# Kernel tuning notes

Measured on AMD Instinct MI355X. Metric: run time of the kernel, lower is better.

## Reference

```python
import jax, jax.numpy as jnp
import numpy as np

USER_NUM = 100000
ITEM_NUM = 50000
EMBED = 64
N_LAYERS = 3
E_RATE = 2000000
E_TRUST = 500000
E_PRED = 100000


def setup_inputs() -> dict:
    key = jax.random.key(0)
    ks = jax.random.split(key, 10)
    return {
        "emb_user": jax.random.normal(ks[0], (USER_NUM, EMBED), dtype=jnp.float32),
        "emb_item": jax.random.normal(ks[1], (ITEM_NUM, EMBED), dtype=jnp.float32),
        "rate_u": jax.random.randint(ks[2], (E_RATE,), 0, USER_NUM, dtype=jnp.int32),
        "rate_i": jax.random.randint(ks[3], (E_RATE,), 0, ITEM_NUM, dtype=jnp.int32),
        "trust_src": jax.random.randint(ks[4], (E_TRUST,), 0, USER_NUM, dtype=jnp.int32),
        "trust_dst": jax.random.randint(ks[5], (E_TRUST,), 0, USER_NUM, dtype=jnp.int32),
        "pos_u": jax.random.randint(ks[6], (E_PRED,), 0, USER_NUM, dtype=jnp.int32),
        "pos_i": jax.random.randint(ks[7], (E_PRED,), 0, ITEM_NUM, dtype=jnp.int32),
        "neg_u": jax.random.randint(ks[8], (E_PRED,), 0, USER_NUM, dtype=jnp.int32),
        "neg_i": jax.random.randint(ks[9], (E_PRED,), 0, ITEM_NUM, dtype=jnp.int32),
    }


def _degrees(idx, n):
    # float degree counts, clamped to >=1 (DGL GraphConv clamps zero degrees)
    d = jax.ops.segment_sum(jnp.ones_like(idx, dtype=jnp.float32), idx, num_segments=n)
    return jnp.maximum(d, 1.0)


def _gcn_conv(h_src, src, dst, n_dst, deg_src, deg_dst):
    # GraphConv(norm='both', weight=False, bias=False):
    # out[v] = deg(v)^-1/2 * sum_{u->v} deg(u)^-1/2 * h[u]
    ns = jax.lax.rsqrt(deg_src)
    nd = jax.lax.rsqrt(deg_dst)
    msg = (h_src * ns[:, None])[src]          # [E, D] gather
    agg = jax.ops.segment_sum(msg, dst, num_segments=n_dst)
    return agg * nd[:, None]


def reference(emb_user, emb_item, rate_u, rate_i, trust_src, trust_dst,
              pos_u, pos_i, neg_u, neg_i):
    nU, nI = emb_user.shape[0], emb_item.shape[0]
    deg_u = _degrees(rate_u, nU)       # user degree in rate graph (out for rate, in for rated-by)
    deg_i = _degrees(rate_i, nI)       # item degree in rate graph
    deg_ts = _degrees(trust_src, nU)
    deg_td = _degrees(trust_dst, nU)

    res_u, res_i = emb_user, emb_item
    cur_u, cur_i = emb_user, emb_item
    for _ in range(N_LAYERS):
        # item -> user ('rated-by'): src deg = deg_i, dst deg = deg_u
        new_u = _gcn_conv(cur_i, rate_i, rate_u, nU, deg_i, deg_u)
        # user -> item ('rate')
        new_i = _gcn_conv(cur_u, rate_u, rate_i, nI, deg_u, deg_i)
        # user -> user ('trust'), added into user output
        new_u = new_u + _gcn_conv(cur_u, trust_src, trust_dst, nU, deg_ts, deg_td)
        res_u = res_u + new_u
        res_i = res_i + new_i
        cur_u, cur_i = new_u, new_i

    scale = 1.0 / (N_LAYERS + 1)
    res_u = res_u * scale
    res_i = res_i * scale

    # HeteroDotProductPredictor on 'rate' etype: u_dot_v -> [E, 1]
    pos_score = jnp.sum(res_u[pos_u] * res_i[pos_i], axis=-1, keepdims=True)
    neg_score = jnp.sum(res_u[neg_u] * res_i[neg_i], axis=-1, keepdims=True)
    return pos_score, neg_score
```

## Files before the change

### kernel.cpp

```cpp
#include <hip/hip_runtime.h>
#include <hip/hip_fp16.h>

#define NU 100000
#define NI 50000
#define D  64
#define CAPU 64
#define CAPI 96
#define CAPT 32
#define BS 256

#define NB1 256
#define KPB1 391
#define CAPB1 9216
#define NB2 256
#define KPB2 196
#define CAPB2 9216
#define NB3 128
#define KPB3 782
#define CAPB3 4864
#define NB4 128
#define CAPB4 4864
#define GR 224
#define GT 32

typedef unsigned long long u64;

__global__ void __launch_bounds__(1024) k_binAll(
    const int* __restrict__ ru, const int* __restrict__ ri,
    const int* __restrict__ ts, const int* __restrict__ td,
    int* __restrict__ bc1, int* __restrict__ bc2,
    int* __restrict__ bc3, int* __restrict__ bc4,
    u64* __restrict__ bins1, u64* __restrict__ bins2,
    u64* __restrict__ bins3, u64* __restrict__ bins4,
    int E_rate, int E_trust)
{
    __shared__ int cnt[512];
    __shared__ int base[512];
    int b = blockIdx.x, tid = threadIdx.x;
    if (b < GR) {
        if (tid < 512) cnt[tid] = 0;
        __syncthreads();
        for (int c0 = b * 1024; c0 < E_rate; c0 += GR * 1024) {
            int e = c0 + tid;
            if (e < E_rate) {
                int u = ru[e], it = ri[e];
                atomicAdd(&cnt[u / KPB1], 1);
                atomicAdd(&cnt[256 + it / KPB2], 1);
            }
        }
        __syncthreads();
        if (tid < 256)      base[tid] = atomicAdd(&bc1[tid], cnt[tid]);
        else if (tid < 512) base[tid] = atomicAdd(&bc2[tid - 256], cnt[tid]);
        __syncthreads();
        if (tid < 512) cnt[tid] = 0;
        __syncthreads();
        for (int c0 = b * 1024; c0 < E_rate; c0 += GR * 1024) {
            int e = c0 + tid;
            if (e < E_rate) {
                int u = ru[e], it = ri[e];
                int b1 = u / KPB1, b2 = it / KPB2;
                int r1 = atomicAdd(&cnt[b1], 1);
                int o1 = base[b1] + r1;
                if (o1 < CAPB1) bins1[(size_t)b1 * CAPB1 + o1] = ((u64)u << 32) | (unsigned)it;
                int r2 = atomicAdd(&cnt[256 + b2], 1);
                int o2 = base[256 + b2] + r2;
                if (o2 < CAPB2) bins2[(size_t)b2 * CAPB2 + o2] = ((u64)it << 32) | (unsigned)u;
            }
        }
    } else {
        int bb = b - GR;
        if (tid < 256) cnt[tid] = 0;
        __syncthreads();
        for (int c0 = bb * 1024; c0 < E_trust; c0 += GT * 1024) {
            int e = c0 + tid;
            if (e < E_trust) {
                int s = ts[e], dd = td[e];
                atomicAdd(&cnt[dd / KPB3], 1);
                atomicAdd(&cnt[128 + s / KPB3], 1);
            }
        }
        __syncthreads();
        if (tid < 128)      base[tid] = atomicAdd(&bc3[tid], cnt[tid]);
        else if (tid < 256) base[tid] = atomicAdd(&bc4[tid - 128], cnt[tid]);
        __syncthreads();
        if (tid < 256) cnt[tid] = 0;
        __syncthreads();
        for (int c0 = bb * 1024; c0 < E_trust; c0 += GT * 1024) {
            int e = c0 + tid;
            if (e < E_trust) {
                int s = ts[e], dd = td[e];
                int b3 = dd / KPB3, b4 = s / KPB3;
                int r3 = atomicAdd(&cnt[b3], 1);
                int o3 = base[b3] + r3;
                if (o3 < CAPB3) bins3[(size_t)b3 * CAPB3 + o3] = ((u64)dd << 32) | (unsigned)s;
                int r4 = atomicAdd(&cnt[128 + b4], 1);
                int o4 = base[128 + b4] + r4;
                if (o4 < CAPB4) bins4[(size_t)b4 * CAPB4 + o4] = ((u64)s << 32);
            }
        }
    }
}

__global__ void __launch_bounds__(512) k_buildAll(
    const u64* __restrict__ bins1, const u64* __restrict__ bins2,
    const u64* __restrict__ bins3, const u64* __restrict__ bins4,
    const int* __restrict__ bc1, const int* __restrict__ bc2,
    const int* __restrict__ bc3, const int* __restrict__ bc4,
    int* __restrict__ colU, int* __restrict__ colI, int* __restrict__ colT,
    int* __restrict__ degU, int* __restrict__ degI,
    int* __restrict__ degT, int* __restrict__ degS)
{
    __shared__ int cnt[KPB3];
    int b = blockIdx.x, tid = threadIdx.x;
    const u64* bins; int n, k0, kpb, colcap, nmax; int* col; int* deg;
    if (b < NB1) {
        bins = bins1 + (size_t)b * CAPB1; n = bc1[b]; if (n > CAPB1) n = CAPB1;
        k0 = b * KPB1; kpb = KPB1; colcap = CAPU; col = colU; deg = degU; nmax = NU;
    } else if (b < NB1 + NB2) {
        int q = b - NB1;
        bins = bins2 + (size_t)q * CAPB2; n = bc2[q]; if (n > CAPB2) n = CAPB2;
        k0 = q * KPB2; kpb = KPB2; colcap = CAPI; col = colI; deg = degI; nmax = NI;
    } else if (b < NB1 + NB2 + NB3) {
        int q = b - NB1 - NB2;
        bins = bins3 + (size_t)q * CAPB3; n = bc3[q]; if (n > CAPB3) n = CAPB3;
        k0 = q * KPB3; kpb = KPB3; colcap = CAPT; col = colT; deg = degT; nmax = NU;
    } else {
        int q = b - NB1 - NB2 - NB3;
        bins = bins4 + (size_t)q * CAPB4; n = bc4[q]; if (n > CAPB4) n = CAPB4;
        k0 = q * KPB3; kpb = KPB3; colcap = 0; col = nullptr; deg = degS; nmax = NU;
    }
    for (int t = tid; t < kpb; t += 512) cnt[t] = 0;
    __syncthreads();
    if (col) {
        for (int i = tid; i < n; i += 512) {
            u64 e = bins[i];
            int k = (int)(e >> 32);
            int v = (int)(e & 0xffffffffu);
            int c = atomicAdd(&cnt[k - k0], 1);
            if (c < colcap) col[(size_t)k * colcap + c] = v;
        }
    } else {
        for (int i = tid; i < n; i += 512) {
            int k = (int)(bins[i] >> 32);
            atomicAdd(&cnt[k - k0], 1);
        }
    }
    __syncthreads();
    for (int t = tid; t < kpb; t += 512) {
        int k = k0 + t;
        if (k < nmax) {
            int c = cnt[t];
            if (colcap && c > colcap) c = colcap;
            deg[k] = c;
        }
    }
}

__global__ void k_degrs(const int* __restrict__ degU, const int* __restrict__ degI,
                        const int* __restrict__ degT, const int* __restrict__ degS,
                        float* __restrict__ rs_u, float* __restrict__ rs_i,
                        float* __restrict__ rs_td, float* __restrict__ rs_tsu) {
    int i = blockIdx.x * blockDim.x + threadIdx.x;
    if (i < NU) {
        int a = degU[i]; float ru = rsqrtf((float)(a < 1 ? 1 : a));
        rs_u[i] = ru;
        int b = degT[i]; rs_td[i] = rsqrtf((float)(b < 1 ? 1 : b));
        int c = degS[i]; rs_tsu[i] = rsqrtf((float)(c < 1 ? 1 : c)) / ru;
    }
    if (i < NI) {
        int a = degI[i]; rs_i[i] = rsqrtf((float)(a < 1 ? 1 : a));
    }
}

__device__ __forceinline__ uint2 pack4(float a, float b, float c, float d) {
    __half2 lo = __floats2half2_rn(a, b);
    __half2 hi = __floats2half2_rn(c, d);
    uint2 r;
    r.x = *(unsigned*)&lo;
    r.y = *(unsigned*)&hi;
    return r;
}

__global__ void k_inith(const float* __restrict__ src, const float* __restrict__ rs,
                        uint2* __restrict__ curS, uint2* __restrict__ res, int n16) {
    int i = blockIdx.x * blockDim.x + threadIdx.x;
    if (i >= n16) return;
    float4 v = ((const float4*)src)[i];
    float s = rs[i >> 4];
    res[i]  = pack4(v.x, v.y, v.z, v.w);
    curS[i] = pack4(s * v.x, s * v.y, s * v.z, s * v.w);
}

__global__ void k_zrow(uint2* uA, uint2* uB, uint2* iA, uint2* iB) {
    int t = threadIdx.x;
    int e = t & 15;
    uint2 z; z.x = 0; z.y = 0;
    if (t < 16)      uA[(size_t)NU * 16 + e] = z;
    else if (t < 32) uB[(size_t)NU * 16 + e] = z;
    else if (t < 48) iA[(size_t)NI * 16 + e] = z;
    else             iB[(size_t)NI * 16 + e] = z;
}

__global__ void k_layer(const int* __restrict__ colU, const int* __restrict__ degU,
                        const int* __restrict__ colT, const int* __restrict__ degT,
                        const int* __restrict__ colI, const int* __restrict__ degI,
                        const float* __restrict__ rs_u, const float* __restrict__ rs_i,
                        const float* __restrict__ rs_td, const float* __restrict__ rs_tsu,
                        const uint2* __restrict__ cuR, const uint2* __restrict__ ciS,
                        uint2* __restrict__ nuR, uint2* __restrict__ niS,
                        uint2* __restrict__ resu, uint2* __restrict__ resi) {
    int b = blockIdx.x;
    int m = b % 3;
    int base = b / 3;
    int wid = threadIdx.x >> 6;
    int lane = threadIdx.x & 63;
    int grp = lane >> 4;
    int gl  = lane & 15;
    if (m < 2) {
        int node = ((base * 2 + m) * 4 + wid) * 4 + grp;
        if (node >= NU) return;
        float4 acc = {0.f, 0.f, 0.f, 0.f};
        {
            int bb = node * CAPU, e = bb + degU[node];
            for (int k0 = bb; k0 < e; k0 += 16) {
                int idx = k0 + gl;
                int n = idx < e ? colU[idx] : NI;
                #pragma unroll
                for (int j = 0; j < 16; ++j) {
                    int nn = __shfl(n, j, 16);
                    uint2 q = ciS[(size_t)nn * 16 + gl];
                    float2 f = __half22float2(*(__half2*)&q.x);
                    float2 g = __half22float2(*(__half2*)&q.y);
                    acc.x += f.x; acc.y += f.y; acc.z += g.x; acc.w += g.y;
                }
            }
        }
        float4 acc2 = {0.f, 0.f, 0.f, 0.f};
        {
            int bb = node * CAPT, e = bb + degT[node];
            int sub = gl & 7;
            for (int k0 = bb; k0 < e; k0 += 8) {
                int idx = k0 + sub;
                int n = idx < e ? colT[idx] : NU;
                float w = idx < e ? rs_tsu[n] : 0.f;
                #pragma unroll
                for (int j = 0; j < 8; ++j) {
                    int nn  = __shfl(n, j, 16);
                    float ww = __shfl(w, j, 16);
                    uint2 q = cuR[(size_t)nn * 16 + gl];
                    float2 f = __half22float2(*(__half2*)&q.x);
                    float2 g = __half22float2(*(__half2*)&q.y);
                    acc2.x += ww * f.x; acc2.y += ww * f.y;
                    acc2.z += ww * g.x; acc2.w += ww * g.y;
                }
            }
        }
        float su = rs_u[node], st = rs_td[node];
        float vx = su * acc.x + st * acc2.x;
        float vy = su * acc.y + st * acc2.y;
        float vz = su * acc.z + st * acc2.z;
        float vw = su * acc.w + st * acc2.w;
        size_t o = (size_t)node * 16 + gl;
        nuR[o] = pack4(su * vx, su * vy, su * vz, su * vw);
        uint2 r = resu[o];
        float2 ra = __half22float2(*(__half2*)&r.x);
        float2 rb = __half22float2(*(__half2*)&r.y);
        resu[o] = pack4(ra.x + vx, ra.y + vy, rb.x + vz, rb.y + vw);
    } else {
        int node = (base * 4 + wid) * 4 + grp;
        if (node >= NI) return;
        float4 acc = {0.f, 0.f, 0.f, 0.f};
        {
            int bb = node * CAPI, e = bb + degI[node];
            for (int k0 = bb; k0 < e; k0 += 16) {
                int idx = k0 + gl;
                int n = idx < e ? colI[idx] : NU;
                #pragma unroll
                for (int j = 0; j < 16; ++j) {
                    int nn = __shfl(n, j, 16);
                    uint2 q = cuR[(size_t)nn * 16 + gl];
                    float2 f = __half22float2(*(__half2*)&q.x);
                    float2 g = __half22float2(*(__half2*)&q.y);
                    acc.x += f.x; acc.y += f.y; acc.z += g.x; acc.w += g.y;
                }
            }
        }
        float si = rs_i[node];
        float vx = si * acc.x, vy = si * acc.y, vz = si * acc.z, vw = si * acc.w;
        size_t o = (size_t)node * 16 + gl;
        niS[o] = pack4(si * vx, si * vy, si * vz, si * vw);
        uint2 r = resi[o];
        float2 ra = __half22float2(*(__half2*)&r.x);
        float2 rb = __half22float2(*(__half2*)&r.y);
        resi[o] = pack4(ra.x + vx, ra.y + vy, rb.x + vz, rb.y + vw);
    }
}

__global__ void k_pred(const int* __restrict__ pu, const int* __restrict__ pi,
                       const int* __restrict__ nuv, const int* __restrict__ niv,
                       const __half2* __restrict__ ru, const __half2* __restrict__ ri,
                       float* __restrict__ out, int E) {
    long long tid = (long long)blockIdx.x * blockDim.x + threadIdx.x;
    int e = (int)(tid >> 4);
    int c2 = ((int)tid & 15) * 2;
    if (e >= 2 * E) return;
    int ee = (e < E) ? e : e - E;
    int u  = (e < E) ? pu[ee] : nuv[ee];
    int it = (e < E) ? pi[ee] : niv[ee];
    float2 a0 = __half22float2(ru[(size_t)u  * 32 + c2]);
    float2 a1 = __half22float2(ru[(size_t)u  * 32 + c2 + 1]);
    float2 b0 = __half22float2(ri[(size_t)it * 32 + c2]);
    float2 b1 = __half22float2(ri[(size_t)it * 32 + c2 + 1]);
    float s = a0.x * b0.x + a0.y * b0.y + a1.x * b1.x + a1.y * b1.y;
    s += __shfl_xor(s, 1); s += __shfl_xor(s, 2);
    s += __shfl_xor(s, 4); s += __shfl_xor(s, 8);
    if (((int)tid & 15) == 0) out[e] = s * (1.0f / 16.0f);
}

extern "C" void kernel_launch(void* const* d_in, const int* in_sizes, int n_in,
                              void* d_out, int out_size, void* d_ws, size_t ws_size,
                              hipStream_t stream) {
    const float* emb_u  = (const float*)d_in[0];
    const float* emb_i  = (const float*)d_in[1];
    const int* rate_u   = (const int*)d_in[2];
    const int* rate_i   = (const int*)d_in[3];
    const int* trust_s  = (const int*)d_in[4];
    const int* trust_d  = (const int*)d_in[5];
    const int* pos_u    = (const int*)d_in[6];
    const int* pos_i    = (const int*)d_in[7];
    const int* neg_u    = (const int*)d_in[8];
    const int* neg_i    = (const int*)d_in[9];
    const int E_rate  = in_sizes[2];
    const int E_trust = in_sizes[4];
    const int E_pred  = in_sizes[6];

    int* iw   = (int*)d_ws;
    int* degU = iw;
    int* degI = degU + NU;
    int* degT = degI + NI;
    int* degS = degT + NU;
    int* bc1  = degS + NU;
    int* bc2  = bc1 + NB1;
    int* bc3  = bc2 + NB2;
    int* bc4  = bc3 + NB3;
    int* colU = bc4 + NB4;
    int* colI = colU + (size_t)NU * CAPU;
    int* colT = colI + (size_t)NI * CAPI;
    float* rs_u   = (float*)(colT + (size_t)NU * CAPT);
    float* rs_i   = rs_u  + NU;
    float* rs_td  = rs_i  + NI;
    float* rs_tsu = rs_td + NU;
    uint2* uRA  = (uint2*)(rs_tsu + NU);
    uint2* uRB  = uRA + (size_t)(NU + 1) * 16;
    uint2* iSA  = uRB + (size_t)(NU + 1) * 16;
    uint2* iSB  = iSA + (size_t)(NI + 1) * 16;
    uint2* res_u = iSB + (size_t)(NI + 1) * 16;
    uint2* res_i = res_u + (size_t)NU * 16;
    u64* bins1 = (u64*)uRA;
    u64* bins2 = bins1 + (size_t)NB1 * CAPB1;
    u64* bins3 = bins2 + (size_t)NB2 * CAPB2;
    u64* bins4 = bins3 + (size_t)NB3 * CAPB3;

    hipMemsetAsync(bc1, 0, (NB1 + NB2 + NB3 + NB4) * sizeof(int), stream);

    k_binAll<<<GR + GT, 1024, 0, stream>>>(rate_u, rate_i, trust_s, trust_d,
                                           bc1, bc2, bc3, bc4,
                                           bins1, bins2, bins3, bins4,
                                           E_rate, E_trust);
    k_buildAll<<<NB1 + NB2 + NB3 + NB4, 512, 0, stream>>>(
        bins1, bins2, bins3, bins4, bc1, bc2, bc3, bc4,
        colU, colI, colT, degU, degI, degT, degS);

    k_degrs<<<(NU + BS - 1) / BS, BS, 0, stream>>>(degU, degI, degT, degS,
                                                   rs_u, rs_i, rs_td, rs_tsu);

    k_inith<<<(NU * 16 + BS - 1) / BS, BS, 0, stream>>>(emb_u, rs_u, uRA, res_u, NU * 16);
    k_inith<<<(NI * 16 + BS - 1) / BS, BS, 0, stream>>>(emb_i, rs_i, iSA, res_i, NI * 16);
    k_zrow<<<1, 64, 0, stream>>>(uRA, uRB, iSA, iSB);

    uint2* cu = uRA; uint2* nu_ = uRB;
    uint2* ci = iSA; uint2* ni_ = iSB;
    for (int l = 0; l < 3; ++l) {
        k_layer<<<9375, BS, 0, stream>>>(colU, degU, colT, degT, colI, degI,
                                         rs_u, rs_i, rs_td, rs_tsu,
                                         cu, ci, nu_, ni_, res_u, res_i);
        uint2* t;
        t = cu; cu = nu_; nu_ = t;
        t = ci; ci = ni_; ni_ = t;
    }

    long long tp = (long long)2 * E_pred * 16;
    k_pred<<<(unsigned)((tp + BS - 1) / BS), BS, 0, stream>>>(
        pos_u, pos_i, neg_u, neg_i, (const __half2*)res_u, (const __half2*)res_i,
        (float*)d_out, E_pred);
}
```

Baseline: 366.3 us.

## Split embeddings into column halves and process layers per half

Reorganises the fp16 node feature arrays into two 32-column halves stored as separate planes. Each layer now runs separate user and item kernels per half, so every gather touches a smaller working set that is more likely to stay in cache. Bin entries are packed into 32-bit words instead of 64-bit, and rating-neighbour sums accumulate in half2 instead of fp32. This trades more launches and repeated index reads for better locality, at the cost of lower accumulation precision.

Result: slower. 465.7 us (+27.1%).

```diff
diff --git a/kernel.cpp b/kernel.cpp
--- a/kernel.cpp
+++ b/kernel.cpp
@@ -3,7 +3,6 @@
 
 #define NU 100000
 #define NI 50000
-#define D  64
 #define CAPU 64
 #define CAPI 96
 #define CAPT 32
@@ -23,15 +22,15 @@
 #define GR 224
 #define GT 32
 
-typedef unsigned long long u64;
+typedef unsigned int u32;
 
 __global__ void __launch_bounds__(1024) k_binAll(
     const int* __restrict__ ru, const int* __restrict__ ri,
     const int* __restrict__ ts, const int* __restrict__ td,
     int* __restrict__ bc1, int* __restrict__ bc2,
     int* __restrict__ bc3, int* __restrict__ bc4,
-    u64* __restrict__ bins1, u64* __restrict__ bins2,
-    u64* __restrict__ bins3, u64* __restrict__ bins4,
+    u32* __restrict__ bins1, u32* __restrict__ bins2,
+    u32* __restrict__ bins3, u32* __restrict__ bins4,
     int E_rate, int E_trust)
 {
     __shared__ int cnt[512];
@@ -61,10 +60,12 @@
                 int b1 = u / KPB1, b2 = it / KPB2;
                 int r1 = atomicAdd(&cnt[b1], 1);
                 int o1 = base[b1] + r1;
-                if (o1 < CAPB1) bins1[(size_t)b1 * CAPB1 + o1] = ((u64)u << 32) | (unsigned)it;
+                if (o1 < CAPB1)
+                    bins1[(size_t)b1 * CAPB1 + o1] = ((u32)(u - b1 * KPB1) << 16) | (u32)it;
                 int r2 = atomicAdd(&cnt[256 + b2], 1);
                 int o2 = base[256 + b2] + r2;
-                if (o2 < CAPB2) bins2[(size_t)b2 * CAPB2 + o2] = ((u64)it << 32) | (unsigned)u;
+                if (o2 < CAPB2)
+                    bins2[(size_t)b2 * CAPB2 + o2] = ((u32)(it - b2 * KPB2) << 17) | (u32)u;
             }
         }
     } else {
@@ -92,18 +93,20 @@
                 int b3 = dd / KPB3, b4 = s / KPB3;
                 int r3 = atomicAdd(&cnt[b3], 1);
                 int o3 = base[b3] + r3;
-                if (o3 < CAPB3) bins3[(size_t)b3 * CAPB3 + o3] = ((u64)dd << 32) | (unsigned)s;
+                if (o3 < CAPB3)
+                    bins3[(size_t)b3 * CAPB3 + o3] = ((u32)(dd - b3 * KPB3) << 17) | (u32)s;
                 int r4 = atomicAdd(&cnt[128 + b4], 1);
                 int o4 = base[128 + b4] + r4;
-                if (o4 < CAPB4) bins4[(size_t)b4 * CAPB4 + o4] = ((u64)s << 32);
+                if (o4 < CAPB4)
+                    bins4[(size_t)b4 * CAPB4 + o4] = (u32)(s - b4 * KPB3);
             }
         }
     }
 }
 
 __global__ void __launch_bounds__(512) k_buildAll(
-    const u64* __restrict__ bins1, const u64* __restrict__ bins2,
-    const u64* __restrict__ bins3, const u64* __restrict__ bins4,
+    const u32* __restrict__ bins1, const u32* __restrict__ bins2,
+    const u32* __restrict__ bins3, const u32* __restrict__ bins4,
     const int* __restrict__ bc1, const int* __restrict__ bc2,
     const int* __restrict__ bc3, const int* __restrict__ bc4,
     int* __restrict__ colU, int* __restrict__ colI, int* __restrict__ colT,
@@ -112,46 +115,71 @@
 {
     __shared__ int cnt[KPB3];
     int b = blockIdx.x, tid = threadIdx.x;
-    const u64* bins; int n, k0, kpb, colcap, nmax; int* col; int* deg;
     if (b < NB1) {
-        bins = bins1 + (size_t)b * CAPB1; n = bc1[b]; if (n > CAPB1) n = CAPB1;
-        k0 = b * KPB1; kpb = KPB1; colcap = CAPU; col = colU; deg = degU; nmax = NU;
+        const u32* bins = bins1 + (size_t)b * CAPB1;
+        int n = bc1[b]; if (n > CAPB1) n = CAPB1;
+        int k0 = b * KPB1;
+        for (int t = tid; t < KPB1; t += 512) cnt[t] = 0;
+        __syncthreads();
+        for (int i = tid; i < n; i += 512) {
+            u32 e = bins[i];
+            int ko = e >> 16, v = e & 0xFFFF;
+            int c = atomicAdd(&cnt[ko], 1);
+            if (c < CAPU) colU[(size_t)(k0 + ko) * CAPU + c] = v;
+        }
+        __syncthreads();
+        for (int t = tid; t < KPB1; t += 512) {
+            int k = k0 + t;
+            if (k < NU) { int c = cnt[t]; if (c > CAPU) c = CAPU; degU[k] = c; }
+        }
     } else if (b < NB1 + NB2) {
         int q = b - NB1;
-        bins = bins2 + (size_t)q * CAPB2; n = bc2[q]; if (n > CAPB2) n = CAPB2;
-        k0 = q * KPB2; kpb = KPB2; colcap = CAPI; col = colI; deg = degI; nmax = NI;
+        const u32* bins = bins2 + (size_t)q * CAPB2;
+        int n = bc2[q]; if (n > CAPB2) n = CAPB2;
+        int k0 = q * KPB2;
+        for (int t = tid; t < KPB2; t += 512) cnt[t] = 0;
+        __syncthreads();
+        for (int i = tid; i < n; i += 512) {
+            u32 e = bins[i];
+            int ko = e >> 17, v = e & 0x1FFFF;
+            int c = atomicAdd(&cnt[ko], 1);
+            if (c < CAPI) colI[(size_t)(k0 + ko) * CAPI + c] = v;
+        }
+        __syncthreads();
+        for (int t = tid; t < KPB2; t += 512) {
+            int k = k0 + t;
+            if (k < NI) { int c = cnt[t]; if (c > CAPI) c = CAPI; degI[k] = c; }
+        }
     } else if (b < NB1 + NB2 + NB3) {
         int q = b - NB1 - NB2;
-        bins = bins3 + (size_t)q * CAPB3; n = bc3[q]; if (n > CAPB3) n = CAPB3;
-        k0 = q * KPB3; kpb = KPB3; colcap = CAPT; col = colT; deg = degT; nmax = NU;
+        const u32* bins = bins3 + (size_t)q * CAPB3;
+        int n = bc3[q]; if (n > CAPB3) n = CAPB3;
+        int k0 = q * KPB3;
+        for (int t = tid; t < KPB3; t += 512) cnt[t] = 0;
+        __syncthreads();
+        for (int i = tid; i < n; i += 512) {
+            u32 e = bins[i];
+            int ko = e >> 17, v = e & 0x1FFFF;
+            int c = atomicAdd(&cnt[ko], 1);
+            if (c < CAPT) colT[(size_t)(k0 + ko) * CAPT + c] = v;
+        }
+        __syncthreads();
+        for (int t = tid; t < KPB3; t += 512) {
+            int k = k0 + t;
+            if (k < NU) { int c = cnt[t]; if (c > CAPT) c = CAPT; degT[k] = c; }
+        }
     } else {
         int q = b - NB1 - NB2 - NB3;
-        bins = bins4 + (size_t)q * CAPB4; n = bc4[q]; if (n > CAPB4) n = CAPB4;
-        k0 = q * KPB3; kpb = KPB3; colcap = 0; col = nullptr; deg = degS; nmax = NU;
-    }
-    for (int t = tid; t < kpb; t += 512) cnt[t] = 0;
-    __syncthreads();
-    if (col) {
-        for (int i = tid; i < n; i += 512) {
-            u64 e = bins[i];
-            int k = (int)(e >> 32);
-            int v = (int)(e & 0xffffffffu);
-            int c = atomicAdd(&cnt[k - k0], 1);
-            if (c < colcap) col[(size_t)k * colcap + c] = v;
-        }
-    } else {
-        for (int i = tid; i < n; i += 512) {
-            int k = (int)(bins[i] >> 32);
-            atomicAdd(&cnt[k - k0], 1);
-        }
-    }
-    __syncthreads();
-    for (int t = tid; t < kpb; t += 512) {
-        int k = k0 + t;
-        if (k < nmax) {
-            int c = cnt[t];
-            if (colcap && c > colcap) c = colcap;
-            deg[k] = c;
+        const u32* bins = bins4 + (size_t)q * CAPB4;
+        int n = bc4[q]; if (n > CAPB4) n = CAPB4;
+        int k0 = q * KPB3;
+        for (int t = tid; t < KPB3; t += 512) cnt[t] = 0;
+        __syncthreads();
+        for (int i = tid; i < n; i += 512) atomicAdd(&cnt[bins[i]], 1);
+        __syncthreads();
+        for (int t = tid; t < KPB3; t += 512) {
+            int k = k0 + t;
+            if (k < NU) degS[k] = cnt[t];
         }
     }
 }
@@ -182,139 +210,147 @@
 }
 
 __global__ void k_inith(const float* __restrict__ src, const float* __restrict__ rs,
-                        uint2* __restrict__ curS, uint2* __restrict__ res, int n16) {
+                        uint2* __restrict__ curS, uint2* __restrict__ res,
+                        int N, int n16) {
     int i = blockIdx.x * blockDim.x + threadIdx.x;
     if (i >= n16) return;
     float4 v = ((const float4*)src)[i];
-    float s = rs[i >> 4];
-    res[i]  = pack4(v.x, v.y, v.z, v.w);
-    curS[i] = pack4(s * v.x, s * v.y, s * v.z, s * v.w);
+    int node = i >> 4, c = i & 15, h = c >> 3, o = c & 7;
+    float s = rs[node];
+    curS[(size_t)h * (N + 1) * 8 + (size_t)node * 8 + o] = pack4(s * v.x, s * v.y, s * v.z, s * v.w);
+    res [(size_t)h * N * 8       + (size_t)node * 8 + o] = pack4(v.x, v.y, v.z, v.w);
 }
 
 __global__ void k_zrow(uint2* uA, uint2* uB, uint2* iA, uint2* iB) {
     int t = threadIdx.x;
-    int e = t & 15;
+    int o = t & 7, h = (t >> 3) & 1;
     uint2 z; z.x = 0; z.y = 0;
-    if (t < 16)      uA[(size_t)NU * 16 + e] = z;
-    else if (t < 32) uB[(size_t)NU * 16 + e] = z;
-    else if (t < 48) iA[(size_t)NI * 16 + e] = z;
-    else             iB[(size_t)NI * 16 + e] = z;
-}
-
-__global__ void k_layer(const int* __restrict__ colU, const int* __restrict__ degU,
+    size_t ou = (size_t)h * (NU + 1) * 8 + (size_t)NU * 8 + o;
+    size_t oi = (size_t)h * (NI + 1) * 8 + (size_t)NI * 8 + o;
+    if (t < 16)      uA[ou] = z;
+    else if (t < 32) uB[ou] = z;
+    else if (t < 48) iA[oi] = z;
+    else             iB[oi] = z;
+}
+
+
+__global__ void k_userh(const int* __restrict__ colU, const int* __restrict__ degU,
                         const int* __restrict__ colT, const int* __restrict__ degT,
-                        const int* __restrict__ colI, const int* __restrict__ degI,
-                        const float* __restrict__ rs_u, const float* __restrict__ rs_i,
-                        const float* __restrict__ rs_td, const float* __restrict__ rs_tsu,
+                        const float* __restrict__ rs_u, const float* __restrict__ rs_td,
+                        const float* __restrict__ rs_tsu,
                         const uint2* __restrict__ cuR, const uint2* __restrict__ ciS,
-                        uint2* __restrict__ nuR, uint2* __restrict__ niS,
-                        uint2* __restrict__ resu, uint2* __restrict__ resi) {
-    int b = blockIdx.x;
-    int m = b % 3;
-    int base = b / 3;
-    int wid = threadIdx.x >> 6;
-    int lane = threadIdx.x & 63;
-    int grp = lane >> 4;
-    int gl  = lane & 15;
-    if (m < 2) {
-        int node = ((base * 2 + m) * 4 + wid) * 4 + grp;
-        if (node >= NU) return;
-        float4 acc = {0.f, 0.f, 0.f, 0.f};
-        {
-            int bb = node * CAPU, e = bb + degU[node];
-            for (int k0 = bb; k0 < e; k0 += 16) {
-                int idx = k0 + gl;
-                int n = idx < e ? colU[idx] : NI;
-                #pragma unroll
-                for (int j = 0; j < 16; ++j) {
-                    int nn = __shfl(n, j, 16);
-                    uint2 q = ciS[(size_t)nn * 16 + gl];
-                    float2 f = __half22float2(*(__half2*)&q.x);
-                    float2 g = __half22float2(*(__half2*)&q.y);
-                    acc.x += f.x; acc.y += f.y; acc.z += g.x; acc.w += g.y;
-                }
-            }
-        }
-        float4 acc2 = {0.f, 0.f, 0.f, 0.f};
-        {
-            int bb = node * CAPT, e = bb + degT[node];
-            int sub = gl & 7;
-            for (int k0 = bb; k0 < e; k0 += 8) {
-                int idx = k0 + sub;
-                int n = idx < e ? colT[idx] : NU;
-                float w = idx < e ? rs_tsu[n] : 0.f;
-                #pragma unroll
-                for (int j = 0; j < 8; ++j) {
-                    int nn  = __shfl(n, j, 16);
-                    float ww = __shfl(w, j, 16);
-                    uint2 q = cuR[(size_t)nn * 16 + gl];
-                    float2 f = __half22float2(*(__half2*)&q.x);
-                    float2 g = __half22float2(*(__half2*)&q.y);
-                    acc2.x += ww * f.x; acc2.y += ww * f.y;
-                    acc2.z += ww * g.x; acc2.w += ww * g.y;
-                }
-            }
-        }
-        float su = rs_u[node], st = rs_td[node];
-        float vx = su * acc.x + st * acc2.x;
-        float vy = su * acc.y + st * acc2.y;
-        float vz = su * acc.z + st * acc2.z;
-        float vw = su * acc.w + st * acc2.w;
-        size_t o = (size_t)node * 16 + gl;
-        nuR[o] = pack4(su * vx, su * vy, su * vz, su * vw);
-        uint2 r = resu[o];
-        float2 ra = __half22float2(*(__half2*)&r.x);
-        float2 rb = __half22float2(*(__half2*)&r.y);
-        resu[o] = pack4(ra.x + vx, ra.y + vy, rb.x + vz, rb.y + vw);
-    } else {
-        int node = (base * 4 + wid) * 4 + grp;
-        if (node >= NI) return;
-        float4 acc = {0.f, 0.f, 0.f, 0.f};
-        {
-            int bb = node * CAPI, e = bb + degI[node];
-            for (int k0 = bb; k0 < e; k0 += 16) {
-                int idx = k0 + gl;
-                int n = idx < e ? colI[idx] : NU;
-                #pragma unroll
-                for (int j = 0; j < 16; ++j) {
-                    int nn = __shfl(n, j, 16);
-                    uint2 q = cuR[(size_t)nn * 16 + gl];
-                    float2 f = __half22float2(*(__half2*)&q.x);
-                    float2 g = __half22float2(*(__half2*)&q.y);
-                    acc.x += f.x; acc.y += f.y; acc.z += g.x; acc.w += g.y;
-                }
-            }
-        }
-        float si = rs_i[node];
-        float vx = si * acc.x, vy = si * acc.y, vz = si * acc.z, vw = si * acc.w;
-        size_t o = (size_t)node * 16 + gl;
-        niS[o] = pack4(si * vx, si * vy, si * vz, si * vw);
-        uint2 r = resi[o];
-        float2 ra = __half22float2(*(__half2*)&r.x);
-        float2 rb = __half22float2(*(__half2*)&r.y);
-        resi[o] = pack4(ra.x + vx, ra.y + vy, rb.x + vz, rb.y + vw);
-    }
+                        uint2* __restrict__ nuR, uint2* __restrict__ resU, int half) {
+    int node = blockIdx.x * 32 + (threadIdx.x >> 3);
+    int gl = threadIdx.x & 7;
+    if (node >= NU) return;
+    const uint2* ciT = ciS + (size_t)half * (NI + 1) * 8;
+    const uint2* cuT = cuR + (size_t)half * (NU + 1) * 8;
+    __half2 ha = __floats2half2_rn(0.f, 0.f), hb = ha;
+    {
+        int bb = node * CAPU, e = bb + degU[node];
+        for (int k0 = bb; k0 < e; k0 += 8) {
+            int idx = k0 + gl;
+            int n = idx < e ? colU[idx] : NI;
+            #pragma unroll
+            for (int j = 0; j < 8; ++j) {
+                int nn = __shfl(n, j, 8);
+                uint2 q = ciT[(size_t)nn * 8 + gl];
+                ha = __hadd2(ha, *(__half2*)&q.x);
+                hb = __hadd2(hb, *(__half2*)&q.y);
+            }
+        }
+    }
+    float2 fa = __half22float2(ha), fb = __half22float2(hb);
+    float4 acc2 = {0.f, 0.f, 0.f, 0.f};
+    {
+        int bb = node * CAPT, e = bb + degT[node];
+        for (int k0 = bb; k0 < e; k0 += 8) {
+            int idx = k0 + gl;
+            int n = idx < e ? colT[idx] : NU;
+            float w = idx < e ? rs_tsu[n] : 0.f;
+            #pragma unroll
+            for (int j = 0; j < 8; ++j) {
+                int nn = __shfl(n, j, 8);
+                float ww = __shfl(w, j, 8);
+                uint2 q = cuT[(size_t)nn * 8 + gl];
+                float2 f = __half22float2(*(__half2*)&q.x);
+                float2 g = __half22float2(*(__half2*)&q.y);
+                acc2.x += ww * f.x; acc2.y += ww * f.y;
+                acc2.z += ww * g.x; acc2.w += ww * g.y;
+            }
+        }
+    }
+    float su = rs_u[node], st = rs_td[node];
+    float vx = su * fa.x + st * acc2.x;
+    float vy = su * fa.y + st * acc2.y;
+    float vz = su * fb.x + st * acc2.z;
+    float vw = su * fb.y + st * acc2.w;
+    size_t oc = (size_t)half * (NU + 1) * 8 + (size_t)node * 8 + gl;
+    nuR[oc] = pack4(su * vx, su * vy, su * vz, su * vw);
+    size_t ro = (size_t)half * NU * 8 + (size_t)node * 8 + gl;
+    uint2 r = resU[ro];
+    float2 ra = __half22float2(*(__half2*)&r.x);
+    float2 rb = __half22float2(*(__half2*)&r.y);
+    resU[ro] = pack4(ra.x + vx, ra.y + vy, rb.x + vz, rb.y + vw);
+}
+
+__global__ void k_itemh(const int* __restrict__ colI, const int* __restrict__ degI,
+                        const float* __restrict__ rs_i,
+                        const uint2* __restrict__ cuR,
+                        uint2* __restrict__ niS, uint2* __restrict__ resI, int half) {
+    int node = blockIdx.x * 32 + (threadIdx.x >> 3);
+    int gl = threadIdx.x & 7;
+    if (node >= NI) return;
+    const uint2* cuT = cuR + (size_t)half * (NU + 1) * 8;
+    __half2 ha = __floats2half2_rn(0.f, 0.f), hb = ha;
+    {
+        int bb = node * CAPI, e = bb + degI[node];
+        for (int k0 = bb; k0 < e; k0 += 8) {
+            int idx = k0 + gl;
+            int n = idx < e ? colI[idx] : NU;
+            #pragma unroll
+            for (int j = 0; j < 8; ++j) {
+                int nn = __shfl(n, j, 8);
+                uint2 q = cuT[(size_t)nn * 8 + gl];
+                ha = __hadd2(ha, *(__half2*)&q.x);
+                hb = __hadd2(hb, *(__half2*)&q.y);
+            }
+        }
+    }
+    float2 fa = __half22float2(ha), fb = __half22float2(hb);
+    float si = rs_i[node];
+    float vx = si * fa.x, vy = si * fa.y, vz = si * fb.x, vw = si * fb.y;
+    size_t oc = (size_t)half * (NI + 1) * 8 + (size_t)node * 8 + gl;
+    niS[oc] = pack4(si * vx, si * vy, si * vz, si * vw);
+    size_t ro = (size_t)half * NI * 8 + (size_t)node * 8 + gl;
+    uint2 r = resI[ro];
+    float2 ra = __half22float2(*(__half2*)&r.x);
+    float2 rb = __half22float2(*(__half2*)&r.y);
+    resI[ro] = pack4(ra.x + vx, ra.y + vy, rb.x + vz, rb.y + vw);
 }
 
 __global__ void k_pred(const int* __restrict__ pu, const int* __restrict__ pi,
                        const int* __restrict__ nuv, const int* __restrict__ niv,
-                       const __half2* __restrict__ ru, const __half2* __restrict__ ri,
+                       const uint2* __restrict__ resU, const uint2* __restrict__ resI,
                        float* __restrict__ out, int E) {
     long long tid = (long long)blockIdx.x * blockDim.x + threadIdx.x;
     int e = (int)(tid >> 4);
-    int c2 = ((int)tid & 15) * 2;
+    int sub = (int)tid & 15;
+    int h = sub >> 3, gl = sub & 7;
     if (e >= 2 * E) return;
     int ee = (e < E) ? e : e - E;
     int u  = (e < E) ? pu[ee] : nuv[ee];
     int it = (e < E) ? pi[ee] : niv[ee];
-    float2 a0 = __half22float2(ru[(size_t)u  * 32 + c2]);
-    float2 a1 = __half22float2(ru[(size_t)u  * 32 + c2 + 1]);
-    float2 b0 = __half22float2(ri[(size_t)it * 32 + c2]);
-    float2 b1 = __half22float2(ri[(size_t)it * 32 + c2 + 1]);
+    uint2 a = resU[(size_t)h * NU * 8 + (size_t)u * 8 + gl];
+    uint2 b = resI[(size_t)h * NI * 8 + (size_t)it * 8 + gl];
+    float2 a0 = __half22float2(*(__half2*)&a.x);
+    float2 a1 = __half22float2(*(__half2*)&a.y);
+    float2 b0 = __half22float2(*(__half2*)&b.x);
+    float2 b1 = __half22float2(*(__half2*)&b.y);
     float s = a0.x * b0.x + a0.y * b0.y + a1.x * b1.x + a1.y * b1.y;
     s += __shfl_xor(s, 1); s += __shfl_xor(s, 2);
     s += __shfl_xor(s, 4); s += __shfl_xor(s, 8);
-    if (((int)tid & 15) == 0) out[e] = s * (1.0f / 16.0f);
+    if (sub == 0) out[e] = s * (1.0f / 16.0f);
 }
 
 extern "C" void kernel_launch(void* const* d_in, const int* in_sizes, int n_in,
@@ -351,15 +387,15 @@
     float* rs_td  = rs_i  + NI;
     float* rs_tsu = rs_td + NU;
     uint2* uRA  = (uint2*)(rs_tsu + NU);
-    uint2* uRB  = uRA + (size_t)(NU + 1) * 16;
-    uint2* iSA  = uRB + (size_t)(NU + 1) * 16;
-    uint2* iSB  = iSA + (size_t)(NI + 1) * 16;
-    uint2* res_u = iSB + (size_t)(NI + 1) * 16;
-    uint2* res_i = res_u + (size_t)NU * 16;
-    u64* bins1 = (u64*)uRA;
-    u64* bins2 = bins1 + (size_t)NB1 * CAPB1;
-    u64* bins3 = bins2 + (size_t)NB2 * CAPB2;
-    u64* bins4 = bins3 + (size_t)NB3 * CAPB3;
+    uint2* uRB  = uRA + (size_t)2 * (NU + 1) * 8;
+    uint2* iSA  = uRB + (size_t)2 * (NU + 1) * 8;
+    uint2* iSB  = iSA + (size_t)2 * (NI + 1) * 8;
+    uint2* resU = iSB + (size_t)2 * (NI + 1) * 8;
+    uint2* resI = resU + (size_t)2 * NU * 8;
+    u32* bins1 = (u32*)uRA;
+    u32* bins2 = bins1 + (size_t)NB1 * CAPB1;
+    u32* bins3 = bins2 + (size_t)NB2 * CAPB2;
+    u32* bins4 = bins3 + (size_t)NB3 * CAPB3;
 
     hipMemsetAsync(bc1, 0, (NB1 + NB2 + NB3 + NB4) * sizeof(int), stream);
 
@@ -374,16 +410,19 @@
     k_degrs<<<(NU + BS - 1) / BS, BS, 0, stream>>>(degU, degI, degT, degS,
                                                    rs_u, rs_i, rs_td, rs_tsu);
 
-    k_inith<<<(NU * 16 + BS - 1) / BS, BS, 0, stream>>>(emb_u, rs_u, uRA, res_u, NU * 16);
-    k_inith<<<(NI * 16 + BS - 1) / BS, BS, 0, stream>>>(emb_i, rs_i, iSA, res_i, NI * 16);
+    k_inith<<<(NU * 16 + BS - 1) / BS, BS, 0, stream>>>(emb_u, rs_u, uRA, resU, NU, NU * 16);
+    k_inith<<<(NI * 16 + BS - 1) / BS, BS, 0, stream>>>(emb_i, rs_i, iSA, resI, NI, NI * 16);
     k_zrow<<<1, 64, 0, stream>>>(uRA, uRB, iSA, iSB);
 
     uint2* cu = uRA; uint2* nu_ = uRB;
     uint2* ci = iSA; uint2* ni_ = iSB;
     for (int l = 0; l < 3; ++l) {
-        k_layer<<<9375, BS, 0, stream>>>(colU, degU, colT, degT, colI, degI,
-                                         rs_u, rs_i, rs_td, rs_tsu,
-                                         cu, ci, nu_, ni_, res_u, res_i);
+        k_userh<<<3125, BS, 0, stream>>>(colU, degU, colT, degT,
+                                         rs_u, rs_td, rs_tsu, cu, ci, nu_, resU, 0);
+        k_itemh<<<1563, BS, 0, stream>>>(colI, degI, rs_i, cu, ni_, resI, 0);
+        k_userh<<<3125, BS, 0, stream>>>(colU, degU, colT, degT,
+                                         rs_u, rs_td, rs_tsu, cu, ci, nu_, resU, 1);
+        k_itemh<<<1563, BS, 0, stream>>>(colI, degI, rs_i, cu, ni_, resI, 1);
         uint2* t;
         t = cu; cu = nu_; nu_ = t;
         t = ci; ci = ni_; ni_ = t;
@@ -391,6 +430,5 @@
 
     long long tp = (long long)2 * E_pred * 16;
     k_pred<<<(unsigned)((tp + BS - 1) / BS), BS, 0, stream>>>(
-        pos_u, pos_i, neg_u, neg_i, (const __half2*)res_u, (const __half2*)res_i,
-        (float*)d_out, E_pred);
-}
+        pos_u, pos_i, neg_u, neg_i, resU, resI, (float*)d_out, E_pred);
+}
```
